# Optimization experiments

Hardware: AMD Instinct MI355X
Metric: run time of the kernel (lower is better)

## Reference

```python
import jax, jax.numpy as jnp
import numpy as np

DIM = 512
D_STATE = 16
D_CONV = 4
EXPAND = 2
D_INNER = EXPAND * DIM
DT_RANK = (DIM + 15) // 16  # ceil(dim/16) = 32
B_SZ, SEQ = 2, 2048


def _silu(v):
    return v * jax.nn.sigmoid(v)


def _mamba(x, in_w, conv_w, conv_b, xproj_w, dt_w, dt_b, A_log, D, out_w):
    """Single Mamba block forward (mamba_ssm reference math).
    x: [B, L, d_model]
    """
    Bb, L, _ = x.shape
    d_inner = conv_w.shape[0]
    d_state = A_log.shape[1]
    dt_rank = dt_w.shape[1]

    xz = x @ in_w.T                          # [B, L, 2*d_inner]
    xi, z = jnp.split(xz, 2, axis=-1)

    # causal depthwise conv1d (kernel D_CONV) + SiLU
    K = conv_w.shape[-1]
    xp = jnp.pad(xi, ((0, 0), (K - 1, 0), (0, 0)))
    xc = conv_b + sum(xp[:, k:k + L, :] * conv_w[:, 0, k] for k in range(K))
    xc = _silu(xc)                           # [B, L, d_inner]

    x_dbl = xc @ xproj_w.T                   # [B, L, dt_rank + 2*d_state]
    dt = x_dbl[..., :dt_rank]
    Bm = x_dbl[..., dt_rank:dt_rank + d_state]
    Cm = x_dbl[..., dt_rank + d_state:]
    dt = jax.nn.softplus(dt @ dt_w.T + dt_b)  # [B, L, d_inner]

    A = -jnp.exp(A_log)                      # [d_inner, d_state]
    dA = jnp.exp(dt[..., None] * A)          # [B, L, d_inner, d_state]
    dBu = (dt * xc)[..., None] * Bm[:, :, None, :]

    def step(h, inp):
        dA_t, dBu_t, C_t = inp
        h = dA_t * h + dBu_t                 # [B, d_inner, d_state]
        y = jnp.einsum('bds,bs->bd', h, C_t)
        return h, y

    h0 = jnp.zeros((Bb, d_inner, d_state), dtype=x.dtype)
    _, ys = jax.lax.scan(
        step, h0,
        (dA.transpose(1, 0, 2, 3), dBu.transpose(1, 0, 2, 3), Cm.transpose(1, 0, 2)))
    y = ys.transpose(1, 0, 2) + D * xc       # skip connection via D
    y = y * _silu(z)
    return y @ out_w.T                       # [B, L, d_model]


def _make_mamba_params(key):
    ks = jax.random.split(key, 7)
    s = 0.02
    in_w = jax.random.normal(ks[0], (2 * D_INNER, DIM), jnp.float32) * s
    conv_w = jax.random.normal(ks[1], (D_INNER, 1, D_CONV), jnp.float32) * 0.2
    conv_b = jnp.zeros((D_INNER,), jnp.float32)
    xproj_w = jax.random.normal(ks[2], (DT_RANK + 2 * D_STATE, D_INNER), jnp.float32) * s
    dt_w = jax.random.normal(ks[3], (D_INNER, DT_RANK), jnp.float32) * (DT_RANK ** -0.5)
    dt_b = jax.random.uniform(ks[4], (D_INNER,), jnp.float32, -4.0, -2.0)  # small softplus(dt)
    A_log = jnp.log(jnp.broadcast_to(jnp.arange(1, D_STATE + 1, dtype=jnp.float32), (D_INNER, D_STATE)))
    D = jnp.ones((D_INNER,), jnp.float32)
    out_w = jax.random.normal(ks[5], (DIM, D_INNER), jnp.float32) * s
    return (in_w, conv_w, conv_b, xproj_w, dt_w, dt_b, A_log, D, out_w)


def setup_inputs() -> dict:
    key = jax.random.key(0)
    kx, kf, kr = jax.random.split(key, 3)
    x = jax.random.normal(kx, (B_SZ, SEQ, DIM), jnp.float32)
    f = _make_mamba_params(kf)
    r = _make_mamba_params(kr)
    names = ['in_w', 'conv_w', 'conv_b', 'xproj_w', 'dt_w', 'dt_b', 'A_log', 'D', 'out_w']
    d = {'x': x}
    for n, v in zip(names, f):
        d['f_' + n] = v
    for n, v in zip(names, r):
        d['r_' + n] = v
    return d


def reference(x,
              f_in_w, f_conv_w, f_conv_b, f_xproj_w, f_dt_w, f_dt_b, f_A_log, f_D, f_out_w,
              r_in_w, r_conv_w, r_conv_b, r_xproj_w, r_dt_w, r_dt_b, r_A_log, r_D, r_out_w):
    x_f = _mamba(x, f_in_w, f_conv_w, f_conv_b, f_xproj_w, f_dt_w, f_dt_b, f_A_log, f_D, f_out_w)
    xr = jnp.flip(x, axis=1)
    x_r = jnp.flip(_mamba(xr, r_in_w, r_conv_w, r_conv_b, r_xproj_w, r_dt_w, r_dt_b, r_A_log, r_D, r_out_w), axis=1)
    return (x_f + x_r) * 0.5
```

## Files before the change

kernel.cpp:

```cpp
#include <hip/hip_runtime.h>
#include <hip/hip_bf16.h>
#include <math.h>

#define DIM      512
#define D_STATE  16
#define D_CONV   4
#define D_INNER  1024
#define DT_RANK  32
#define B_SZ     2
#define SEQ      2048
#define NTOK     (B_SZ * SEQ)
#define CHUNK    64
#define NCH      (SEQ / CHUNK)
#define NC_PAD   1152
#define PG       8
#define NPG      (CHUNK / PG)

#define XCB_STR   4194304
#define WCB_STR   1179648
#define BC_STR    131072
#define CH_STR    1048576

typedef __attribute__((ext_vector_type(8))) short bf16x8;
typedef __attribute__((ext_vector_type(4))) float f32x4;

__device__ __forceinline__ short f2bf(float f) {
    unsigned u = __float_as_uint(f);
    u += 0x7fffu + ((u >> 16) & 1u);
    return (short)(u >> 16);
}
__device__ __forceinline__ float bf2f(short v) {
    return __uint_as_float(((unsigned)(unsigned short)v) << 16);
}
__device__ __forceinline__ float softplus_fast(float v) {
    return (v > 20.f) ? v : __logf(1.f + __expf(v));
}

__global__ __launch_bounds__(256)
void cvt_bf16(const float* __restrict__ src, short* __restrict__ dst, int n)
{
    int i = (blockIdx.x * 256 + threadIdx.x) * 8;
    if (i >= n) return;
    float4 a = *(const float4*)(src + i);
    float4 b = *(const float4*)(src + i + 4);
    bf16x8 v;
    v[0] = f2bf(a.x); v[1] = f2bf(a.y); v[2] = f2bf(a.z); v[3] = f2bf(a.w);
    v[4] = f2bf(b.x); v[5] = f2bf(b.y); v[6] = f2bf(b.z); v[7] = f2bf(b.w);
    *(bf16x8*)(dst + i) = v;
}

__global__ __launch_bounds__(256)
void cvt_wcat(const float* __restrict__ wf, const float* __restrict__ wr,
              short* __restrict__ Wcat)
{
    int idx = blockIdx.x * 256 + threadIdx.x;
    if (idx >= 512 * 2048) return;
    int n = idx >> 11, col = idx & 2047;
    const float* src = (col < 1024) ? wf : wr;
    Wcat[idx] = f2bf(src[n * 1024 + (col & 1023)]);
}

__global__ __launch_bounds__(256)
void build_wc(const float* __restrict__ xp0, const float* __restrict__ xp1,
              const float* __restrict__ dw0, const float* __restrict__ dw1,
              short* __restrict__ Wcb)
{
    const int dir = blockIdx.y;
    int idx = blockIdx.x * 256 + threadIdx.x;
    if (idx >= NC_PAD * D_INNER) return;
    const float* xproj_w = dir ? xp1 : xp0;
    const float* dt_w    = dir ? dw1 : dw0;
    int i = idx >> 10, k = idx & 1023;
    float v;
    if (i < 1024) {
        v = 0.f;
#pragma unroll
        for (int r = 0; r < 32; ++r)
            v = fmaf(dt_w[i * 32 + r], xproj_w[r * 1024 + k], v);
    } else if (i < 1056) {
        v = xproj_w[(i - 1024 + 32) * 1024 + k];
    } else {
        v = 0.f;
    }
    Wcb[(size_t)dir * WCB_STR + idx] = f2bf(v);
}

#define TM 128
#define TN 128
#define TK 32

__global__ __launch_bounds__(256)
void gemm_bf16(const short* __restrict__ A, const short* __restrict__ A2,
               int lda, int K1,
               const short* __restrict__ W, int ldw,
               void* __restrict__ Cv, int ldc,
               int K, float alpha, int cmode,
               const float* __restrict__ dtb0, const float* __restrict__ dtb1,
               float* __restrict__ BCb, int aStr, int wStr)
{
    __shared__ __align__(16) short As[2][TM * TK];
    __shared__ __align__(16) short Ws[2][TN * TK];

    const int nx = gridDim.x, ny = gridDim.y;
    const int nwg = nx * ny * gridDim.z;
    int lin = blockIdx.x + nx * (blockIdx.y + ny * blockIdx.z);
    int swz = (lin & 7) * (nwg >> 3) + (lin >> 3);
    const int bx = swz % nx;
    int tmp = swz / nx;
    const int by = tmp % ny;
    const int dir = tmp / ny;

    A  += (size_t)dir * aStr;
    A2 += (size_t)dir * aStr;
    W  += (size_t)dir * wStr;

    const int tid  = threadIdx.x;
    const int lane = tid & 63;
    const int wid  = tid >> 6;
    const int wr   = wid >> 1, wc = wid & 1;
    const int m0 = by * TM;
    const int n0 = bx * TN;

    const int am0 = ((tid >> 6) << 4) | (tid & 15);
    const int kc0 = (tid >> 4) & 3;
    const size_t arow0 = (size_t)(m0 + am0) * lda + kc0 * 8;
    const size_t arow1 = arow0 + (size_t)64 * lda;
    const short* pw0 = W + (size_t)(n0 + am0) * ldw + kc0 * 8;
    const short* pw1 = pw0 + (size_t)64 * ldw;

    const int ci0 = tid, ci1 = tid + 256;

    f32x4 acc[4][4] = {};
    const int nt = K / TK;

    bf16x8 ra0, ra1, rw0, rw1;

#define LOADR(tt) do {                                          \
    const int off_ = (tt) * TK;                                 \
    const short* ab_ = (off_ < K1) ? A : A2;                    \
    const int ao_ = (off_ < K1) ? off_ : off_ - K1;             \
    ra0 = *(const bf16x8*)(ab_ + arow0 + ao_);                  \
    ra1 = *(const bf16x8*)(ab_ + arow1 + ao_);                  \
    rw0 = *(const bf16x8*)(pw0 + off_);                         \
    rw1 = *(const bf16x8*)(pw1 + off_); } while (0)

#define DSWRITE(buf) do {                                       \
    *(bf16x8*)(As[buf] + ci0 * 8) = ra0;                        \
    *(bf16x8*)(As[buf] + ci1 * 8) = ra1;                        \
    *(bf16x8*)(Ws[buf] + ci0 * 8) = rw0;                        \
    *(bf16x8*)(Ws[buf] + ci1 * 8) = rw1; } while (0)

    LOADR(0);
    DSWRITE(0);
    LOADR(1);
    __syncthreads();

    for (int t = 0; t < nt; ++t) {
        const int cur = t & 1;
        if (t + 1 < nt) DSWRITE(cur ^ 1);
        if (t + 2 < nt) LOADR(t + 2);

        bf16x8 af[4], bff[4];
#pragma unroll
        for (int f = 0; f < 4; ++f) {
            int ai = (wr * 4 + f) * 64 + (lane >> 4) * 16 + (lane & 15);
            af[f]  = *(const bf16x8*)(&As[cur][ai * 8]);
            int bi = (wc * 4 + f) * 64 + (lane >> 4) * 16 + (lane & 15);
            bff[f] = *(const bf16x8*)(&Ws[cur][bi * 8]);
        }
#pragma unroll
        for (int i = 0; i < 4; ++i)
#pragma unroll
            for (int j = 0; j < 4; ++j)
                acc[i][j] = __builtin_amdgcn_mfma_f32_16x16x32_bf16(
                    af[i], bff[j], acc[i][j], 0, 0, 0);
        __syncthreads();
    }
#undef LOADR
#undef DSWRITE

    if (cmode == 2) {
        short* C = (short*)Cv;
#pragma unroll
        for (int i = 0; i < 4; ++i) {
            int row = m0 + wr * 64 + i * 16 + ((lane >> 4) << 2);
#pragma unroll
            for (int j = 0; j < 4; ++j) {
                int col = n0 + wc * 64 + j * 16 + (lane & 15);
#pragma unroll
                for (int r = 0; r < 4; ++r)
                    C[(size_t)(row + r) * ldc + col] = f2bf(alpha * acc[i][j][r]);
            }
        }
    } else if (cmode == 3) {
        if (n0 < 1024) {
            short* dtO = (short*)Cv;
            const float* dtb = dir ? dtb1 : dtb0;
#pragma unroll
            for (int i = 0; i < 4; ++i) {
                int row = m0 + wr * 64 + i * 16 + ((lane >> 4) << 2);
#pragma unroll
                for (int j = 0; j < 4; ++j) {
                    int col = n0 + wc * 64 + j * 16 + (lane & 15);
                    float bias = dtb[col];
#pragma unroll
                    for (int r = 0; r < 4; ++r) {
                        float v = softplus_fast(acc[i][j][r] + bias);
                        dtO[(size_t)(row + r) * 4096 + dir * 2048 + col] = f2bf(v);
                    }
                }
            }
        } else {
            float* bc = BCb + (size_t)dir * BC_STR;
#pragma unroll
            for (int i = 0; i < 4; ++i) {
                int row = m0 + wr * 64 + i * 16 + ((lane >> 4) << 2);
#pragma unroll
                for (int j = 0; j < 4; ++j) {
                    int col = n0 + wc * 64 + j * 16 + (lane & 15);
                    if (col < 1056) {
#pragma unroll
                        for (int r = 0; r < 4; ++r)
                            bc[(size_t)(row + r) * 32 + (col - 1024)] = acc[i][j][r];
                    }
                }
            }
        }
    } else {
        float* C = (float*)Cv;
#pragma unroll
        for (int i = 0; i < 4; ++i) {
            int row = m0 + wr * 64 + i * 16 + ((lane >> 4) << 2);
#pragma unroll
            for (int j = 0; j < 4; ++j) {
                int col = n0 + wc * 64 + j * 16 + (lane & 15);
#pragma unroll
                for (int r = 0; r < 4; ++r)
                    C[(size_t)(row + r) * ldc + col] = alpha * acc[i][j][r];
            }
        }
    }
}

__global__ __launch_bounds__(256)
void conv_silu_kernel(const short* __restrict__ xzb,
                      const float* __restrict__ cw0, const float* __restrict__ cw1,
                      const float* __restrict__ cb0, const float* __restrict__ cb1,
                      short* __restrict__ xcb)
{
    const int rev = blockIdx.y;
    int idx = blockIdx.x * 256 + threadIdx.x;
    if (idx >= NTOK * D_INNER) return;
    int c   = idx & (D_INNER - 1);
    int row = idx >> 10;
    int b   = row / SEQ;
    int u   = row - b * SEQ;
    const int coff = rev * 2048 + c;
    const float* cw = rev ? cw1 : cw0;
    const float* cb = rev ? cb1 : cb0;

    float w0 = cw[c * 4 + 0], w1 = cw[c * 4 + 1];
    float w2 = cw[c * 4 + 2], w3 = cw[c * 4 + 3];
    float accv = cb[c];
    if (!rev) {
#pragma unroll
        for (int k = 0; k < 4; ++k) {
            int uu = u - 3 + k;
            float wv = (k == 0) ? w0 : (k == 1) ? w1 : (k == 2) ? w2 : w3;
            if (uu >= 0)
                accv = fmaf(wv, bf2f(xzb[(size_t)(b * SEQ + uu) * 4096 + coff]), accv);
        }
    } else {
#pragma unroll
        for (int k = 0; k < 4; ++k) {
            int uu = u + 3 - k;
            float wv = (k == 0) ? w0 : (k == 1) ? w1 : (k == 2) ? w2 : w3;
            if (uu < SEQ)
                accv = fmaf(wv, bf2f(xzb[(size_t)(b * SEQ + uu) * 4096 + coff]), accv);
        }
    }
    float r = accv / (1.f + __expf(-accv));
    xcb[(size_t)rev * XCB_STR + idx] = f2bf(r);
}

__global__ __launch_bounds__(256)
void scan_p1(const short* __restrict__ xzb,
             const short* __restrict__ xcb,
             const float* __restrict__ BCb,
             const float* __restrict__ A_log0, const float* __restrict__ A_log1,
             float* __restrict__ chP, float* __restrict__ chH)
{
    __shared__ float Bs[CHUNK][16];
    const int tid = threadIdx.x;
    const int blk = blockIdx.x;
    const int dir = blk >> 8;
    const int rr  = blk & 255;
    const int cb = rr & 3;
    const int ch = (rr >> 2) & (NCH - 1);
    const int b  = rr >> 7;
    const int c  = cb * 256 + tid;
    const int rev = dir;

    const int u0 = rev ? (SEQ - 1 - ch * CHUNK) : (ch * CHUNK);
    const int st = rev ? -1 : 1;
    const float* A_log = dir ? A_log1 : A_log0;
    const float* bcD = BCb + (size_t)dir * BC_STR;

    for (int r = tid; r < CHUNK * 16; r += 256) {
        int i = r >> 4, s = r & 15;
        int row = b * SEQ + u0 + st * i;
        Bs[i][s] = bcD[(size_t)row * 32 + s];
    }

    float Acs[16];
#pragma unroll
    for (int s = 0; s < 16; ++s)
        Acs[s] = -__expf(A_log[c * 16 + s]) * 1.44269504f;

    float h[16], P[16];
#pragma unroll
    for (int s = 0; s < 16; ++s) { h[s] = 0.f; P[s] = 1.f; }

    __syncthreads();

    const short* dtp = xzb + (size_t)(b * SEQ + u0) * 4096 + dir * 2048 + c;
    const short* xcp = xcb + (size_t)dir * XCB_STR + (size_t)(b * SEQ + u0) * D_INNER + c;
    const ptrdiff_t dstep = (ptrdiff_t)st * 4096;
    const ptrdiff_t xstep = (ptrdiff_t)st * D_INNER;

    float dt_r[PG], xc_r[PG];
#pragma unroll
    for (int j = 0; j < PG; ++j) {
        dt_r[j] = bf2f(dtp[dstep * j]);
        xc_r[j] = bf2f(xcp[xstep * j]);
    }

#pragma unroll 1
    for (int g = 0; g < NPG; ++g) {
        const int gg = (g + 1 < NPG) ? (g + 1) : g;
        float dt_n[PG], xc_n[PG];
#pragma unroll
        for (int j = 0; j < PG; ++j) {
            int i = gg * PG + j;
            dt_n[j] = bf2f(dtp[dstep * i]);
            xc_n[j] = bf2f(xcp[xstep * i]);
        }
#pragma unroll
        for (int j = 0; j < PG; ++j) {
            int i = g * PG + j;
            float dtv = dt_r[j];
            float e = dtv * xc_r[j];
#pragma unroll
            for (int s = 0; s < 16; ++s) {
                float da = __builtin_amdgcn_exp2f(dtv * Acs[s]);
                h[s] = fmaf(da, h[s], e * Bs[i][s]);
                P[s] *= da;
            }
        }
#pragma unroll
        for (int j = 0; j < PG; ++j) { dt_r[j] = dt_n[j]; xc_r[j] = xc_n[j]; }
    }

    size_t o = (size_t)dir * CH_STR + ((size_t)(b * NCH + ch) * 1024 + c) * 16;
#pragma unroll
    for (int q = 0; q < 4; ++q) {
        *(float4*)&chP[o + q * 4] = make_float4(P[q*4], P[q*4+1], P[q*4+2], P[q*4+3]);
        *(float4*)&chH[o + q * 4] = make_float4(h[q*4], h[q*4+1], h[q*4+2], h[q*4+3]);
    }
}

__global__ __launch_bounds__(256)
void scan_p2(float* __restrict__ chPH, const float* __restrict__ chH)
{
    int idx = blockIdx.x * 256 + threadIdx.x;
    int dir = idx >> 15;
    int rem = idx & 32767;
    int b  = rem >> 14;
    int cs = rem & 16383;
    size_t base = (size_t)dir * CH_STR;
    float h = 0.f;
#pragma unroll
    for (int ch = 0; ch < NCH; ++ch) {
        size_t o = base + ((size_t)(b * NCH + ch) << 14) + cs;
        float Pv = chPH[o], Hv = chH[o];
        chPH[o] = h;
        h = fmaf(Pv, h, Hv);
    }
}

__global__ __launch_bounds__(256)
void scan_p3(const short* __restrict__ xzb,
             short* __restrict__ xcb,
             const float* __restrict__ BCb,
             const float* __restrict__ A_log0, const float* __restrict__ A_log1,
             const float* __restrict__ Dp0, const float* __restrict__ Dp1,
             const float* __restrict__ hst)
{
    __shared__ float Bs[CHUNK][16];
    __shared__ float Cs[CHUNK][16];
    const int tid = threadIdx.x;
    const int blk = blockIdx.x;
    const int dir = blk >> 8;
    const int rr  = blk & 255;
    const int cb = rr & 3;
    const int ch = (rr >> 2) & (NCH - 1);
    const int b  = rr >> 7;
    const int c  = cb * 256 + tid;
    const int rev = dir;

    const int u0 = rev ? (SEQ - 1 - ch * CHUNK) : (ch * CHUNK);
    const int st = rev ? -1 : 1;
    const float* A_log = dir ? A_log1 : A_log0;
    const float* Dp    = dir ? Dp1 : Dp0;
    const float* bcD = BCb + (size_t)dir * BC_STR;

    for (int r = tid; r < CHUNK * 16; r += 256) {
        int i = r >> 4, s = r & 15;
        int row = b * SEQ + u0 + st * i;
        Bs[i][s] = bcD[(size_t)row * 32 + s];
        Cs[i][s] = bcD[(size_t)row * 32 + 16 + s];
    }

    float Acs[16];
#pragma unroll
    for (int s = 0; s < 16; ++s)
        Acs[s] = -__expf(A_log[c * 16 + s]) * 1.44269504f;

    const float Dc = Dp[c];

    float h[16];
    size_t o = (size_t)dir * CH_STR + ((size_t)(b * NCH + ch) * 1024 + c) * 16;
#pragma unroll
    for (int q = 0; q < 4; ++q) {
        float4 hv = *(const float4*)&hst[o + q * 4];
        h[q*4] = hv.x; h[q*4+1] = hv.y; h[q*4+2] = hv.z; h[q*4+3] = hv.w;
    }

    __syncthreads();

    const short* dtp = xzb + (size_t)(b * SEQ + u0) * 4096 + dir * 2048 + c;
    const short* zp  = xzb + (size_t)(b * SEQ + u0) * 4096 + dir * 2048 + 1024 + c;
    short*       xcp = xcb + (size_t)dir * XCB_STR + (size_t)(b * SEQ + u0) * D_INNER + c;
    const ptrdiff_t dstep = (ptrdiff_t)st * 4096;
    const ptrdiff_t xstep = (ptrdiff_t)st * D_INNER;

    float dt_r[PG], xc_r[PG], z_r[PG];
#pragma unroll
    for (int j = 0; j < PG; ++j) {
        dt_r[j] = bf2f(dtp[dstep * j]);
        xc_r[j] = bf2f(xcp[xstep * j]);
        z_r[j]  = bf2f(zp[dstep * j]);
    }

#pragma unroll 1
    for (int g = 0; g < NPG; ++g) {
        const int gg = (g + 1 < NPG) ? (g + 1) : g;
        float dt_n[PG], xc_n[PG], z_n[PG];
#pragma unroll
        for (int j = 0; j < PG; ++j) {
            int i = gg * PG + j;
            dt_n[j] = bf2f(dtp[dstep * i]);
            xc_n[j] = bf2f(xcp[xstep * i]);
            z_n[j]  = bf2f(zp[dstep * i]);
        }
#pragma unroll
        for (int j = 0; j < PG; ++j) {
            int i = g * PG + j;
            float dtv = dt_r[j];
            float xcv = xc_r[j];
            float e = dtv * xcv;
            float y = 0.f;
#pragma unroll
            for (int s = 0; s < 16; ++s) {
                float da = __builtin_amdgcn_exp2f(dtv * Acs[s]);
                h[s] = fmaf(da, h[s], e * Bs[i][s]);
                y = fmaf(h[s], Cs[i][s], y);
            }
            y = fmaf(Dc, xcv, y);
            float zv = z_r[j];
            float sig = 1.f / (1.f + __expf(-zv));
            xcp[xstep * i] = f2bf(y * zv * sig);
        }
#pragma unroll
        for (int j = 0; j < PG; ++j) {
            dt_r[j] = dt_n[j]; xc_r[j] = xc_n[j]; z_r[j] = z_n[j];
        }
    }
}

extern "C" void kernel_launch(void* const* d_in, const int* in_sizes, int n_in,
                              void* d_out, int out_size, void* d_ws, size_t ws_size,
                              hipStream_t stream)
{
    const float* x = (const float*)d_in[0];
    float* out = (float*)d_out;
    float* ws  = (float*)d_ws;

    short* xzb  = (short*)ws;
    float* BCb  = ws + 8388608;
    float* chP  = ws + 8650752;
    float* chH  = ws + 10747904;
    short* Wcb  = (short*)(ws + 12845056);
    short* xbf  = (short*)(ws + 14024704);
    short* W1b  = (short*)(ws + 15073280);
    short* Wcat = (short*)(ws + 16121856);
    short* xcb  = (short*)(ws + 16646144);

    const int gElem = (NTOK * D_INNER + 255) / 256;

    cvt_bf16<<<(NTOK * DIM / 8 + 255) / 256, 256, 0, stream>>>(x, xbf, NTOK * DIM);
    cvt_bf16<<<(2 * D_INNER * DIM / 8 + 255) / 256, 256, 0, stream>>>(
        (const float*)d_in[1 + 0 * 9 + 0], W1b, 2 * D_INNER * DIM);
    cvt_bf16<<<(2 * D_INNER * DIM / 8 + 255) / 256, 256, 0, stream>>>(
        (const float*)d_in[1 + 1 * 9 + 0], W1b + 2 * D_INNER * DIM, 2 * D_INNER * DIM);
    cvt_wcat<<<(512 * 2048 + 255) / 256, 256, 0, stream>>>(
        (const float*)d_in[1 + 0 * 9 + 8], (const float*)d_in[1 + 1 * 9 + 8], Wcat);
    {
        dim3 g((NC_PAD * D_INNER + 255) / 256, 2);
        build_wc<<<g, 256, 0, stream>>>(
            (const float*)d_in[1 + 0 * 9 + 3], (const float*)d_in[1 + 1 * 9 + 3],
            (const float*)d_in[1 + 0 * 9 + 4], (const float*)d_in[1 + 1 * 9 + 4],
            Wcb);
    }

    {
        dim3 g(4096 / TN, NTOK / TM, 1);
        gemm_bf16<<<g, 256, 0, stream>>>(xbf, xbf, DIM, DIM, W1b, DIM,
                                         xzb, 4096, DIM, 1.f, 2,
                                         nullptr, nullptr, nullptr, 0, 0);
    }
    {
        dim3 g(gElem, 2);
        conv_silu_kernel<<<g, 256, 0, stream>>>(
            xzb,
            (const float*)d_in[1 + 0 * 9 + 1], (const float*)d_in[1 + 1 * 9 + 1],
            (const float*)d_in[1 + 0 * 9 + 2], (const float*)d_in[1 + 1 * 9 + 2],
            xcb);
    }
    {
        dim3 g(NC_PAD / TN, NTOK / TM, 2);
        gemm_bf16<<<g, 256, 0, stream>>>(xcb, xcb, D_INNER, D_INNER,
                                         Wcb, D_INNER,
                                         xzb, 0, D_INNER, 1.f, 3,
                                         (const float*)d_in[1 + 0 * 9 + 5],
                                         (const float*)d_in[1 + 1 * 9 + 5],
                                         BCb, XCB_STR, WCB_STR);
    }
    scan_p1<<<512, 256, 0, stream>>>(xzb, xcb, BCb,
                                     (const float*)d_in[1 + 0 * 9 + 6],
                                     (const float*)d_in[1 + 1 * 9 + 6],
                                     chP, chH);
    scan_p2<<<(2 * B_SZ * 16384) / 256, 256, 0, stream>>>(chP, chH);
    scan_p3<<<512, 256, 0, stream>>>(xzb, xcb, BCb,
                                     (const float*)d_in[1 + 0 * 9 + 6],
                                     (const float*)d_in[1 + 1 * 9 + 6],
                                     (const float*)d_in[1 + 0 * 9 + 7],
                                     (const float*)d_in[1 + 1 * 9 + 7],
                                     chP);
    {
        dim3 g(DIM / TN, NTOK / TM, 1);
        gemm_bf16<<<g, 256, 0, stream>>>(xcb, xcb + XCB_STR, D_INNER, D_INNER,
                                         Wcat, 2 * D_INNER,
                                         out, DIM, 2 * D_INNER, 0.5f, 0,
                                         nullptr, nullptr, nullptr, 0, 0);
    }
}
```

Baseline: 266.5 us.

## Add 64x64 GEMM tile variant for output projection and derive chunk decay from dt sum

Templates the bf16 GEMM with a second configuration (64x64 output tile, K-tile 64) and uses it for the final output projection, whose 512-column output gave only 128 workgroups with 128x128 tiles. The smaller tile gives four times as many workgroups to fill the GPU, at the cost of less data reuse per tile. Separately, the chunk scan no longer multiplies 16 per-step decay products. It accumulates the sum of dt and computes each state's chunk decay once as exp2(A*sum dt), removing a multiply per state per step at a slight change in floating-point rounding.

```diff
diff --git a/kernel.cpp b/kernel.cpp
--- a/kernel.cpp
+++ b/kernel.cpp
@@ -85,10 +85,7 @@
     Wcb[(size_t)dir * WCB_STR + idx] = f2bf(v);
 }
 
-#define TM 128
-#define TN 128
-#define TK 32
-
+template<int CFG>
 __global__ __launch_bounds__(256)
 void gemm_bf16(const short* __restrict__ A, const short* __restrict__ A2,
                int lda, int K1,
@@ -98,8 +95,12 @@
                const float* __restrict__ dtb0, const float* __restrict__ dtb1,
                float* __restrict__ BCb, int aStr, int wStr)
 {
-    __shared__ __align__(16) short As[2][TM * TK];
-    __shared__ __align__(16) short Ws[2][TN * TK];
+    constexpr int TMc = CFG ? 64 : 128;
+    constexpr int TKc = CFG ? 64 : 32;
+    constexpr int WTS = CFG ? 32 : 64;
+    constexpr int FC  = CFG ? 2 : 4;
+    __shared__ __align__(16) short As[2][TMc * TKc];
+    __shared__ __align__(16) short Ws[2][TMc * TKc];
 
     const int nx = gridDim.x, ny = gridDim.y;
     const int nwg = nx * ny * gridDim.z;
@@ -118,25 +119,27 @@
     const int lane = tid & 63;
     const int wid  = tid >> 6;
     const int wr   = wid >> 1, wc = wid & 1;
-    const int m0 = by * TM;
-    const int n0 = bx * TN;
-
-    const int am0 = ((tid >> 6) << 4) | (tid & 15);
-    const int kc0 = (tid >> 4) & 3;
+    const int m0 = by * TMc;
+    const int n0 = bx * TMc;
+
+    const int am0 = CFG ? (((tid >> 7) << 4) | (tid & 15))
+                        : (((tid >> 6) << 4) | (tid & 15));
+    const int kc0 = CFG ? ((tid >> 4) & 7) : ((tid >> 4) & 3);
+    const int rstep = CFG ? 32 : 64;
     const size_t arow0 = (size_t)(m0 + am0) * lda + kc0 * 8;
-    const size_t arow1 = arow0 + (size_t)64 * lda;
+    const size_t arow1 = arow0 + (size_t)rstep * lda;
     const short* pw0 = W + (size_t)(n0 + am0) * ldw + kc0 * 8;
-    const short* pw1 = pw0 + (size_t)64 * ldw;
+    const short* pw1 = pw0 + (size_t)rstep * ldw;
 
     const int ci0 = tid, ci1 = tid + 256;
 
-    f32x4 acc[4][4] = {};
-    const int nt = K / TK;
+    f32x4 acc[FC][FC] = {};
+    const int nt = K / TKc;
 
     bf16x8 ra0, ra1, rw0, rw1;
 
 #define LOADR(tt) do {                                          \
-    const int off_ = (tt) * TK;                                 \
+    const int off_ = (tt) * TKc;                                \
     const short* ab_ = (off_ < K1) ? A : A2;                    \
     const int ao_ = (off_ < K1) ? off_ : off_ - K1;             \
     ra0 = *(const bf16x8*)(ab_ + arow0 + ao_);                  \
@@ -160,20 +163,42 @@
         if (t + 1 < nt) DSWRITE(cur ^ 1);
         if (t + 2 < nt) LOADR(t + 2);
 
-        bf16x8 af[4], bff[4];
-#pragma unroll
-        for (int f = 0; f < 4; ++f) {
-            int ai = (wr * 4 + f) * 64 + (lane >> 4) * 16 + (lane & 15);
-            af[f]  = *(const bf16x8*)(&As[cur][ai * 8]);
-            int bi = (wc * 4 + f) * 64 + (lane >> 4) * 16 + (lane & 15);
-            bff[f] = *(const bf16x8*)(&Ws[cur][bi * 8]);
-        }
-#pragma unroll
-        for (int i = 0; i < 4; ++i)
-#pragma unroll
-            for (int j = 0; j < 4; ++j)
-                acc[i][j] = __builtin_amdgcn_mfma_f32_16x16x32_bf16(
-                    af[i], bff[j], acc[i][j], 0, 0, 0);
+        if constexpr (CFG == 0) {
+            bf16x8 af[4], bff[4];
+#pragma unroll
+            for (int f = 0; f < 4; ++f) {
+                int ai = (wr * 4 + f) * 64 + (lane >> 4) * 16 + (lane & 15);
+                af[f]  = *(const bf16x8*)(&As[cur][ai * 8]);
+                int bi = (wc * 4 + f) * 64 + (lane >> 4) * 16 + (lane & 15);
+                bff[f] = *(const bf16x8*)(&Ws[cur][bi * 8]);
+            }
+#pragma unroll
+            for (int i = 0; i < 4; ++i)
+#pragma unroll
+                for (int j = 0; j < 4; ++j)
+                    acc[i][j] = __builtin_amdgcn_mfma_f32_16x16x32_bf16(
+                        af[i], bff[j], acc[i][j], 0, 0, 0);
+        } else {
+            bf16x8 af[2][2], bff[2][2];
+#pragma unroll
+            for (int f = 0; f < 2; ++f)
+#pragma unroll
+                for (int ks = 0; ks < 2; ++ks) {
+                    int ai = (wr * 2 + f) * 128 + ks * 64 + (lane >> 4) * 16 + (lane & 15);
+                    af[f][ks] = *(const bf16x8*)(&As[cur][ai * 8]);
+                    int bi = (wc * 2 + f) * 128 + ks * 64 + (lane >> 4) * 16 + (lane & 15);
+                    bff[f][ks] = *(const bf16x8*)(&Ws[cur][bi * 8]);
+                }
+#pragma unroll
+            for (int i = 0; i < 2; ++i)
+#pragma unroll
+                for (int j = 0; j < 2; ++j) {
+                    acc[i][j] = __builtin_amdgcn_mfma_f32_16x16x32_bf16(
+                        af[i][0], bff[j][0], acc[i][j], 0, 0, 0);
+                    acc[i][j] = __builtin_amdgcn_mfma_f32_16x16x32_bf16(
+                        af[i][1], bff[j][1], acc[i][j], 0, 0, 0);
+                }
+        }
         __syncthreads();
     }
 #undef LOADR
@@ -182,11 +207,11 @@
     if (cmode == 2) {
         short* C = (short*)Cv;
 #pragma unroll
-        for (int i = 0; i < 4; ++i) {
-            int row = m0 + wr * 64 + i * 16 + ((lane >> 4) << 2);
-#pragma unroll
-            for (int j = 0; j < 4; ++j) {
-                int col = n0 + wc * 64 + j * 16 + (lane & 15);
+        for (int i = 0; i < FC; ++i) {
+            int row = m0 + wr * WTS + i * 16 + ((lane >> 4) << 2);
+#pragma unroll
+            for (int j = 0; j < FC; ++j) {
+                int col = n0 + wc * WTS + j * 16 + (lane & 15);
 #pragma unroll
                 for (int r = 0; r < 4; ++r)
                     C[(size_t)(row + r) * ldc + col] = f2bf(alpha * acc[i][j][r]);
@@ -197,11 +222,11 @@
             short* dtO = (short*)Cv;
             const float* dtb = dir ? dtb1 : dtb0;
 #pragma unroll
-            for (int i = 0; i < 4; ++i) {
-                int row = m0 + wr * 64 + i * 16 + ((lane >> 4) << 2);
-#pragma unroll
-                for (int j = 0; j < 4; ++j) {
-                    int col = n0 + wc * 64 + j * 16 + (lane & 15);
+            for (int i = 0; i < FC; ++i) {
+                int row = m0 + wr * WTS + i * 16 + ((lane >> 4) << 2);
+#pragma unroll
+                for (int j = 0; j < FC; ++j) {
+                    int col = n0 + wc * WTS + j * 16 + (lane & 15);
                     float bias = dtb[col];
 #pragma unroll
                     for (int r = 0; r < 4; ++r) {
@@ -213,11 +238,11 @@
         } else {
             float* bc = BCb + (size_t)dir * BC_STR;
 #pragma unroll
-            for (int i = 0; i < 4; ++i) {
-                int row = m0 + wr * 64 + i * 16 + ((lane >> 4) << 2);
-#pragma unroll
-                for (int j = 0; j < 4; ++j) {
-                    int col = n0 + wc * 64 + j * 16 + (lane & 15);
+            for (int i = 0; i < FC; ++i) {
+                int row = m0 + wr * WTS + i * 16 + ((lane >> 4) << 2);
+#pragma unroll
+                for (int j = 0; j < FC; ++j) {
+                    int col = n0 + wc * WTS + j * 16 + (lane & 15);
                     if (col < 1056) {
 #pragma unroll
                         for (int r = 0; r < 4; ++r)
@@ -229,11 +254,11 @@
     } else {
         float* C = (float*)Cv;
 #pragma unroll
-        for (int i = 0; i < 4; ++i) {
-            int row = m0 + wr * 64 + i * 16 + ((lane >> 4) << 2);
-#pragma unroll
-            for (int j = 0; j < 4; ++j) {
-                int col = n0 + wc * 64 + j * 16 + (lane & 15);
+        for (int i = 0; i < FC; ++i) {
+            int row = m0 + wr * WTS + i * 16 + ((lane >> 4) << 2);
+#pragma unroll
+            for (int j = 0; j < FC; ++j) {
+                int col = n0 + wc * WTS + j * 16 + (lane & 15);
 #pragma unroll
                 for (int r = 0; r < 4; ++r)
                     C[(size_t)(row + r) * ldc + col] = alpha * acc[i][j][r];
@@ -317,9 +342,10 @@
     for (int s = 0; s < 16; ++s)
         Acs[s] = -__expf(A_log[c * 16 + s]) * 1.44269504f;
 
-    float h[16], P[16];
-#pragma unroll
-    for (int s = 0; s < 16; ++s) { h[s] = 0.f; P[s] = 1.f; }
+    float h[16];
+    float dts = 0.f;
+#pragma unroll
+    for (int s = 0; s < 16; ++s) h[s] = 0.f;
 
     __syncthreads();
 
@@ -350,11 +376,11 @@
             int i = g * PG + j;
             float dtv = dt_r[j];
             float e = dtv * xc_r[j];
+            dts += dtv;
 #pragma unroll
             for (int s = 0; s < 16; ++s) {
                 float da = __builtin_amdgcn_exp2f(dtv * Acs[s]);
                 h[s] = fmaf(da, h[s], e * Bs[i][s]);
-                P[s] *= da;
             }
         }
 #pragma unroll
@@ -364,7 +390,12 @@
     size_t o = (size_t)dir * CH_STR + ((size_t)(b * NCH + ch) * 1024 + c) * 16;
 #pragma unroll
     for (int q = 0; q < 4; ++q) {
-        *(float4*)&chP[o + q * 4] = make_float4(P[q*4], P[q*4+1], P[q*4+2], P[q*4+3]);
+        float4 pv;
+        pv.x = __builtin_amdgcn_exp2f(Acs[q*4+0] * dts);
+        pv.y = __builtin_amdgcn_exp2f(Acs[q*4+1] * dts);
+        pv.z = __builtin_amdgcn_exp2f(Acs[q*4+2] * dts);
+        pv.w = __builtin_amdgcn_exp2f(Acs[q*4+3] * dts);
+        *(float4*)&chP[o + q * 4] = pv;
         *(float4*)&chH[o + q * 4] = make_float4(h[q*4], h[q*4+1], h[q*4+2], h[q*4+3]);
     }
 }
@@ -524,10 +555,10 @@
     }
 
     {
-        dim3 g(4096 / TN, NTOK / TM, 1);
-        gemm_bf16<<<g, 256, 0, stream>>>(xbf, xbf, DIM, DIM, W1b, DIM,
-                                         xzb, 4096, DIM, 1.f, 2,
-                                         nullptr, nullptr, nullptr, 0, 0);
+        dim3 g(4096 / 128, NTOK / 128, 1);
+        gemm_bf16<0><<<g, 256, 0, stream>>>(xbf, xbf, DIM, DIM, W1b, DIM,
+                                            xzb, 4096, DIM, 1.f, 2,
+                                            nullptr, nullptr, nullptr, 0, 0);
     }
     {
         dim3 g(gElem, 2);
@@ -538,13 +569,13 @@
             xcb);
     }
     {
-        dim3 g(NC_PAD / TN, NTOK / TM, 2);
-        gemm_bf16<<<g, 256, 0, stream>>>(xcb, xcb, D_INNER, D_INNER,
-                                         Wcb, D_INNER,
-                                         xzb, 0, D_INNER, 1.f, 3,
-                                         (const float*)d_in[1 + 0 * 9 + 5],
-                                         (const float*)d_in[1 + 1 * 9 + 5],
-                                         BCb, XCB_STR, WCB_STR);
+        dim3 g(NC_PAD / 128, NTOK / 128, 2);
+        gemm_bf16<0><<<g, 256, 0, stream>>>(xcb, xcb, D_INNER, D_INNER,
+                                            Wcb, D_INNER,
+                                            xzb, 0, D_INNER, 1.f, 3,
+                                            (const float*)d_in[1 + 0 * 9 + 5],
+                                            (const float*)d_in[1 + 1 * 9 + 5],
+                                            BCb, XCB_STR, WCB_STR);
     }
     scan_p1<<<512, 256, 0, stream>>>(xzb, xcb, BCb,
                                      (const float*)d_in[1 + 0 * 9 + 6],
@@ -558,10 +589,10 @@
                                      (const float*)d_in[1 + 1 * 9 + 7],
                                      chP);
     {
-        dim3 g(DIM / TN, NTOK / TM, 1);
-        gemm_bf16<<<g, 256, 0, stream>>>(xcb, xcb + XCB_STR, D_INNER, D_INNER,
-                                         Wcat, 2 * D_INNER,
-                                         out, DIM, 2 * D_INNER, 0.5f, 0,
-                                         nullptr, nullptr, nullptr, 0, 0);
-    }
-}
+        dim3 g(DIM / 64, NTOK / 64, 1);
+        gemm_bf16<1><<<g, 256, 0, stream>>>(xcb, xcb + XCB_STR, D_INNER, D_INNER,
+                                            Wcat, 2 * D_INNER,
+                                            out, DIM, 2 * D_INNER, 0.5f, 0,
+                                            nullptr, nullptr, nullptr, 0, 0);
+    }
+}
```

Result: faster. 253.8 us (median of 3 runs) (-4.8%).
